# Kernel tuning notes

Hardware: AMD Instinct MI355X
Metric: run time of the kernel (lower is better)

## Reference

```python
import jax, jax.numpy as jnp
import numpy as np

# Bit-slice widths from SliceMethod([1,2,4]) on both input and weight sides
# (MSB-first, 7 magnitude bits total, sign carried per-element in each slice).
IN_SLICES = (1, 2, 4)
W_SLICES = (1, 2, 4)


def _l2norm(a):
    # F.normalize(a, p=2, dim=1)
    n = jnp.sqrt(jnp.sum(a * a, axis=1, keepdims=True))
    return a / jnp.maximum(n, 1e-12)


def _quantize(a, nbits):
    # symmetric fixed-point quantization to `nbits` magnitude bits,
    # dynamic per-tensor scale (bw_e=None -> fixed-point path)
    Q = float(2 ** nbits - 1)
    scale = jnp.max(jnp.abs(a))
    q = jnp.round(a / scale * Q)  # integer-valued float32 in [-Q, Q]
    return q, scale / Q


def _bit_slices(q, widths):
    # split |q| into bit groups (MSB-first per slice_method order); sign is
    # folded into each slice so recombination sum_k 2^off_k * slice_k == q
    sign = jnp.sign(q)
    mag = jnp.abs(q)
    total = sum(widths)
    slices = []
    off = total
    for w in widths:
        off -= w
        s = jnp.mod(jnp.floor(mag / (2.0 ** off)), 2.0 ** w)
        slices.append((sign * s, off))
    return slices


def setup_inputs() -> dict:
    key = jax.random.key(0)
    kx, kw = jax.random.split(key)
    x = jax.random.normal(kx, (4096, 1024), dtype=jnp.float32)
    weight = jax.random.normal(kw, (8192, 1024), dtype=jnp.float32)  # vectors.t -> [M, D]
    return {"x": x, "weight": weight}


def reference(x, weight):
    xn = _l2norm(x)        # [B, D]
    wn = _l2norm(weight)   # [M, D]
    qx, sx = _quantize(xn, sum(IN_SLICES))
    qw, sw = _quantize(wn, sum(W_SLICES))
    x_slices = _bit_slices(qx, IN_SLICES)
    w_slices = _bit_slices(qw, W_SLICES)
    # map_reduce_dot_func: 9 slice-pair low-bit GEMMs, recombined with 2^(oi+oj)
    acc = jnp.zeros((x.shape[0], weight.shape[0]), dtype=jnp.float32)
    for xs_k, ox in x_slices:
        for ws_k, ow in w_slices:
            acc = acc + (2.0 ** (ox + ow)) * jnp.einsum('bd,md->bm', xs_k, ws_k)
    cos = acc * sx * sw  # dequantize -> cosine similarity in [-1, 1]
    return 1.0 - cos
```

## Files before the change

### kernel.cpp

```cpp
#include <hip/hip_runtime.h>
#include <cstdint>
#include <cstddef>


#define D_COLS 1024
#define M_ROWS 4096
#define N_ROWS 8192

using i32x4 = __attribute__((ext_vector_type(4))) int;

__device__ __forceinline__ void gload_lds16(const void* g, void* lds) {
  __builtin_amdgcn_global_load_lds(
      (const __attribute__((address_space(1))) uint32_t*)g,
      (__attribute__((address_space(3))) uint32_t*)lds, 16, 0, 0);
}

__global__ __launch_bounds__(256) void rownorm_kernel(
    const float* __restrict__ x, const float* __restrict__ w,
    float* __restrict__ invnorm, float* __restrict__ rmax) {
  const int row = blockIdx.x;
  const float* a = (row < M_ROWS) ? x + (size_t)row * D_COLS
                                  : w + (size_t)(row - M_ROWS) * D_COLS;
  const float4 v = ((const float4*)a)[threadIdx.x];
  float ss = v.x * v.x + v.y * v.y + v.z * v.z + v.w * v.w;
  float mx = fmaxf(fmaxf(fabsf(v.x), fabsf(v.y)), fmaxf(fabsf(v.z), fabsf(v.w)));
#pragma unroll
  for (int off = 32; off; off >>= 1) {
    ss += __shfl_down(ss, off, 64);
    mx = fmaxf(mx, __shfl_down(mx, off, 64));
  }
  __shared__ float s_ss[4], s_mx[4];
  const int wave = threadIdx.x >> 6, lane = threadIdx.x & 63;
  if (lane == 0) { s_ss[wave] = ss; s_mx[wave] = mx; }
  __syncthreads();
  if (threadIdx.x == 0) {
    float tss = (s_ss[0] + s_ss[1]) + (s_ss[2] + s_ss[3]);
    float tmx = fmaxf(fmaxf(s_mx[0], s_mx[1]), fmaxf(s_mx[2], s_mx[3]));
    float inv = 1.0f / fmaxf(sqrtf(tss), 1e-12f);
    invnorm[row] = inv;
    rmax[row] = tmx * inv;
  }
}

__global__ __launch_bounds__(1024) void scale_reduce_kernel(
    const float* __restrict__ rmax, float* __restrict__ scales) {
  const int t = threadIdx.x;
  float mx = 0.f, mw = 0.f;
  for (int i = t; i < M_ROWS; i += 1024) mx = fmaxf(mx, rmax[i]);
  for (int i = t; i < N_ROWS; i += 1024) mw = fmaxf(mw, rmax[M_ROWS + i]);
#pragma unroll
  for (int off = 32; off; off >>= 1) {
    mx = fmaxf(mx, __shfl_down(mx, off, 64));
    mw = fmaxf(mw, __shfl_down(mw, off, 64));
  }
  __shared__ float smx[16], smw[16];
  const int wave = t >> 6, lane = t & 63;
  if (lane == 0) { smx[wave] = mx; smw[wave] = mw; }
  __syncthreads();
  if (t == 0) {
    float a = 0.f, b = 0.f;
#pragma unroll
    for (int i = 0; i < 16; ++i) { a = fmaxf(a, smx[i]); b = fmaxf(b, smw[i]); }
    scales[0] = a;
    scales[1] = b;
  }
}

__global__ __launch_bounds__(256) void quant_transpose_kernel(
    const float* __restrict__ a, const float* __restrict__ invnorm,
    const float* __restrict__ scale, uint4* __restrict__ img) {
  __shared__ uint4 T[128][16];
  const int t = threadIdx.x;
  const int g = blockIdx.x & 3;
  const int rh = (blockIdx.x >> 2) & 1;
  const int p = blockIdx.x >> 3;
  const float s = 127.0f / scale[0];

  const int cc_l = t & 15;
  const int tr = t >> 4;
#pragma unroll
  for (int rc = 0; rc < 8; ++rc) {
    const int rl = rc * 16 + tr;
    const int r = p * 256 + rh * 128 + rl;
    const float f = invnorm[r] * s;
    const float4* src = (const float4*)(a + (size_t)r * D_COLS + (g * 16 + cc_l) * 16);
    unsigned pk[4];
#pragma unroll
    for (int q = 0; q < 4; ++q) {
      const float4 v = src[q];
      const int q0 = (int)rintf(v.x * f), q1 = (int)rintf(v.y * f);
      const int q2 = (int)rintf(v.z * f), q3 = (int)rintf(v.w * f);
      pk[q] = (unsigned)(q0 & 0xff) | ((unsigned)(q1 & 0xff) << 8) |
              ((unsigned)(q2 & 0xff) << 16) | ((unsigned)(q3 & 0xff) << 24);
    }
    T[rl][cc_l ^ (rl & 15)] = make_uint4(pk[0], pk[1], pk[2], pk[3]);
  }
  __syncthreads();

  const int cc_w = t >> 4;
  const int rw = t & 15;
  uint4* dst = img + (size_t)p * 16384 + (size_t)(g * 16 + cc_w) * 256 + rh * 128;
#pragma unroll
  for (int i = 0; i < 8; ++i) {
    const int rl = i * 16 + rw;
    dst[rl] = T[rl][cc_w ^ (rl & 15)];
  }
}

__global__ __launch_bounds__(512, 2) void gemm_i8_kernel(
    const char* __restrict__ qx, const char* __restrict__ qw,
    const float* __restrict__ sx, const float* __restrict__ sw,
    float* __restrict__ out) {
  __shared__ __align__(16) char L[131072];
  const int t = threadIdx.x;
  const int wave = t >> 6, lane = t & 63;
  const int wr = wave >> 2, wc = wave & 3;
  const int rl = lane & 15, ko = lane >> 4;

  i32x4 acc[8][4] = {};

#define ISSUE_HT(h)                                                           \
  {                                                                           \
    const int kt_ = (h) >> 1, ks_ = (h) & 1, bb_ = (h) & 3;                   \
    const char* sa_ = qx + ((size_t)blockIdx.y * 8 + kt_) * 32768 + ks_ * 16384; \
    const char* sb_ = qw + ((size_t)blockIdx.x * 8 + kt_) * 32768 + ks_ * 16384; \
    _Pragma("unroll") for (int i_ = 0; i_ < 2; ++i_) {                        \
      gload_lds16(sa_ + wave * 2048 + i_ * 1024 + lane * 16,                  \
                  L + bb_ * 32768 + wave * 2048 + i_ * 1024);                 \
      gload_lds16(sb_ + wave * 2048 + i_ * 1024 + lane * 16,                  \
                  L + bb_ * 32768 + 16384 + wave * 2048 + i_ * 1024);         \
    }                                                                         \
  }

#define PHASE(h, VM)                                                          \
  {                                                                           \
    if ((h) + 3 < 16) ISSUE_HT((h) + 3);                                      \
    asm volatile("s_waitcnt vmcnt(" #VM ")" ::: "memory");                    \
    asm volatile("s_barrier" ::: "memory");                                   \
    const char* Ab_ = L + ((h) & 3) * 32768;                                  \
    const char* Bb_ = Ab_ + 16384;                                            \
    i32x4 af_[8], bf_[4];                                                     \
    _Pragma("unroll") for (int m_ = 0; m_ < 8; ++m_)                          \
      af_[m_] = *(const i32x4*)(Ab_ + (ko * 256 + wr * 128 + m_ * 16 + rl) * 16); \
    _Pragma("unroll") for (int n_ = 0; n_ < 4; ++n_)                          \
      bf_[n_] = *(const i32x4*)(Bb_ + (ko * 256 + wc * 64 + n_ * 16 + rl) * 16); \
    __builtin_amdgcn_s_setprio(1);                                            \
    _Pragma("unroll") for (int m_ = 0; m_ < 8; ++m_)                          \
      _Pragma("unroll") for (int n_ = 0; n_ < 4; ++n_)                        \
        acc[m_][n_] = __builtin_amdgcn_mfma_i32_16x16x64_i8(                  \
            af_[m_], bf_[n_], acc[m_][n_], 0, 0, 0);                          \
    __builtin_amdgcn_s_setprio(0);                                            \
    asm volatile("s_barrier" ::: "memory");                                   \
  }

  ISSUE_HT(0);
  ISSUE_HT(1);
  ISSUE_HT(2);

#pragma unroll 1
  for (int h = 0; h < 13; ++h) PHASE(h, 12);
  PHASE(13, 8);
  PHASE(14, 4);
  PHASE(15, 0);
#undef PHASE
#undef ISSUE_HT

  const float cs = sx[0] * sw[0] * (1.0f / 16129.0f);
  const int rowBase = blockIdx.y * 256;
  const int colBase = blockIdx.x * 256;
#pragma unroll
  for (int m = 0; m < 8; ++m) {
    const int row = rowBase + wr * 128 + m * 16 + ko * 4;
#pragma unroll
    for (int n = 0; n < 4; ++n) {
      const int col = colBase + wc * 64 + n * 16 + rl;
#pragma unroll
      for (int j = 0; j < 4; ++j)
        out[(size_t)(row + j) * N_ROWS + col] = 1.0f - (float)acc[m][n][j] * cs;
    }
  }
}

extern "C" void kernel_launch(void* const* d_in, const int* in_sizes, int n_in,
                              void* d_out, int out_size, void* d_ws, size_t ws_size,
                              hipStream_t stream) {
  const float* x = (const float*)d_in[0];
  const float* w = (const float*)d_in[1];
  float* out = (float*)d_out;

  char* ws = (char*)d_ws;
  char* qx = ws;
  char* qw = ws + (size_t)M_ROWS * D_COLS;
  float* invnorm = (float*)(ws + (size_t)(M_ROWS + N_ROWS) * D_COLS);
  float* rmax = invnorm + (M_ROWS + N_ROWS);
  float* scales = rmax + (M_ROWS + N_ROWS);

  rownorm_kernel<<<M_ROWS + N_ROWS, 256, 0, stream>>>(x, w, invnorm, rmax);
  scale_reduce_kernel<<<1, 1024, 0, stream>>>(rmax, scales);

  quant_transpose_kernel<<<M_ROWS / 256 * 8, 256, 0, stream>>>(
      x, invnorm, &scales[0], (uint4*)qx);
  quant_transpose_kernel<<<N_ROWS / 256 * 8, 256, 0, stream>>>(
      w, invnorm + M_ROWS, &scales[1], (uint4*)qw);

  dim3 grid(N_ROWS / 256, M_ROWS / 256);
  gemm_i8_kernel<<<grid, 512, 0, stream>>>(qx, qw, &scales[0], &scales[1], out);
}
```

Measured before the change: 80.82 us.

## Restructure int8 GEMM mainloop into double-buffered K-tiles with quarter-phase interleaving

Replaces the 4-deep ring of half-K-tiles with a 2-buffer scheme holding full 32KB K-tiles for A and B. Each K-tile is split into four phases that each issue half the MFMAs, and the next tile's global-to-LDS loads are spread across the first two phases. B fragments are reused across phase pairs and the min-waves-per-EU hint of 2 is dropped. The goal is to interleave loads with compute at finer granularity and cut register pressure. In exchange the prefetch depth drops to one tile, and the extra barriers per tile could expose memory latency.

Result: no change. 81.72 us (+1.1%).

```diff
diff --git a/kernel.cpp b/kernel.cpp
--- a/kernel.cpp
+++ b/kernel.cpp
@@ -107,7 +107,7 @@
   }
 }
 
-__global__ __launch_bounds__(512, 2) void gemm_i8_kernel(
+__global__ __launch_bounds__(512) void gemm_i8_kernel(
     const char* __restrict__ qx, const char* __restrict__ qw,
     const float* __restrict__ sx, const float* __restrict__ sw,
     float* __restrict__ out) {
@@ -119,51 +119,61 @@
 
   i32x4 acc[8][4] = {};
 
-#define ISSUE_HT(h)                                                           \
+#define ISSUE_PART(kt, part)                                                  \
   {                                                                           \
-    const int kt_ = (h) >> 1, ks_ = (h) & 1, bb_ = (h) & 3;                   \
-    const char* sa_ = qx + ((size_t)blockIdx.y * 8 + kt_) * 32768 + ks_ * 16384; \
-    const char* sb_ = qw + ((size_t)blockIdx.x * 8 + kt_) * 32768 + ks_ * 16384; \
-    _Pragma("unroll") for (int i_ = 0; i_ < 2; ++i_) {                        \
-      gload_lds16(sa_ + wave * 2048 + i_ * 1024 + lane * 16,                  \
-                  L + bb_ * 32768 + wave * 2048 + i_ * 1024);                 \
-      gload_lds16(sb_ + wave * 2048 + i_ * 1024 + lane * 16,                  \
-                  L + bb_ * 32768 + 16384 + wave * 2048 + i_ * 1024);         \
+    const char* sa_ = qx + ((size_t)blockIdx.y * 8 + (kt)) * 32768;           \
+    const char* sb_ = qw + ((size_t)blockIdx.x * 8 + (kt)) * 32768;           \
+    char* d_ = L + ((kt) & 1) * 65536;                                        \
+    _Pragma("unroll") for (int i_ = (part) * 2; i_ < (part) * 2 + 2; ++i_) {  \
+      gload_lds16(sa_ + wave * 4096 + i_ * 1024 + lane * 16,                  \
+                  d_ + wave * 4096 + i_ * 1024);                              \
+      gload_lds16(sb_ + wave * 4096 + i_ * 1024 + lane * 16,                  \
+                  d_ + 32768 + wave * 4096 + i_ * 1024);                      \
     }                                                                         \
   }
 
-#define PHASE(h, VM)                                                          \
+#define PHASE(kt, f)                                                          \
   {                                                                           \
-    if ((h) + 3 < 16) ISSUE_HT((h) + 3);                                      \
-    asm volatile("s_waitcnt vmcnt(" #VM ")" ::: "memory");                    \
-    asm volatile("s_barrier" ::: "memory");                                   \
-    const char* Ab_ = L + ((h) & 3) * 32768;                                  \
-    const char* Bb_ = Ab_ + 16384;                                            \
-    i32x4 af_[8], bf_[4];                                                     \
-    _Pragma("unroll") for (int m_ = 0; m_ < 8; ++m_)                          \
-      af_[m_] = *(const i32x4*)(Ab_ + (ko * 256 + wr * 128 + m_ * 16 + rl) * 16); \
-    _Pragma("unroll") for (int n_ = 0; n_ < 4; ++n_)                          \
-      bf_[n_] = *(const i32x4*)(Bb_ + (ko * 256 + wc * 64 + n_ * 16 + rl) * 16); \
+    const char* Ab_ = L + ((kt) & 1) * 65536;                                 \
+    const char* Bb_ = Ab_ + 32768;                                            \
+    const int kh_ = (f) >> 1, qm_ = (f) & 1;                                  \
+    i32x4 af_[4];                                                             \
+    _Pragma("unroll") for (int m_ = 0; m_ < 4; ++m_)                          \
+      af_[m_] = *(const i32x4*)(Ab_ +                                         \
+          ((kh_ * 4 + ko) * 256 + wr * 128 + qm_ * 64 + m_ * 16 + rl) * 16);  \
+    if ((f) % 2 == 0) {                                                       \
+      _Pragma("unroll") for (int n_ = 0; n_ < 4; ++n_)                        \
+        bf_[n_] = *(const i32x4*)(Bb_ +                                       \
+            ((kh_ * 4 + ko) * 256 + wc * 64 + n_ * 16 + rl) * 16);            \
+    }                                                                         \
+    if ((kt) < 7 && (f) < 2) ISSUE_PART((kt) + 1, (f));                       \
+    if ((f) == 3) asm volatile("s_waitcnt vmcnt(0)" ::: "memory");            \
+    __builtin_amdgcn_s_barrier();                                             \
+    asm volatile("s_waitcnt lgkmcnt(0)" ::: "memory");                        \
     __builtin_amdgcn_s_setprio(1);                                            \
-    _Pragma("unroll") for (int m_ = 0; m_ < 8; ++m_)                          \
+    _Pragma("unroll") for (int m_ = 0; m_ < 4; ++m_)                          \
       _Pragma("unroll") for (int n_ = 0; n_ < 4; ++n_)                        \
-        acc[m_][n_] = __builtin_amdgcn_mfma_i32_16x16x64_i8(                  \
-            af_[m_], bf_[n_], acc[m_][n_], 0, 0, 0);                          \
+        acc[qm_ * 4 + m_][n_] = __builtin_amdgcn_mfma_i32_16x16x64_i8(        \
+            af_[m_], bf_[n_], acc[qm_ * 4 + m_][n_], 0, 0, 0);                \
     __builtin_amdgcn_s_setprio(0);                                            \
-    asm volatile("s_barrier" ::: "memory");                                   \
-  }
-
-  ISSUE_HT(0);
-  ISSUE_HT(1);
-  ISSUE_HT(2);
+    __builtin_amdgcn_s_barrier();                                             \
+  }
+
+  ISSUE_PART(0, 0);
+  ISSUE_PART(0, 1);
+  asm volatile("s_waitcnt vmcnt(0)" ::: "memory");
+  __builtin_amdgcn_s_barrier();
 
 #pragma unroll 1
-  for (int h = 0; h < 13; ++h) PHASE(h, 12);
-  PHASE(13, 8);
-  PHASE(14, 4);
-  PHASE(15, 0);
+  for (int kt = 0; kt < 8; ++kt) {
+    i32x4 bf_[4];
+    PHASE(kt, 0);
+    PHASE(kt, 1);
+    PHASE(kt, 2);
+    PHASE(kt, 3);
+  }
 #undef PHASE
-#undef ISSUE_HT
+#undef ISSUE_PART
 
   const float cs = sx[0] * sw[0] * (1.0f / 16129.0f);
   const int rowBase = blockIdx.y * 256;
```

## Shrink GEMM tile to 128x128 with 4 waves, double buffering and XCD swizzle

Applied to the files above, without the earlier changes.

The int8 GEMM moves from 256x256 tiles with 8 waves and a 4-deep LDS ring (128KB) to 128x128 tiles with 4 waves and a 2-stage 32KB LDS buffer, aiming for 3 blocks per CU. The 1D grid of 2048 blocks is swizzled so consecutive block IDs spread across XCDs. The quant/transpose kernel's output layout is changed to match the new 128-row K-slab packing. Smaller tiles halve data reuse per block, raising global/L2 traffic, and the shallower prefetch exposes more load latency, in exchange for more blocks in flight.

Measured after the change: 88.13 us. +9.0%, slower.

```diff
diff --git a/kernel.cpp b/kernel.cpp
--- a/kernel.cpp
+++ b/kernel.cpp
@@ -72,8 +72,7 @@
   __shared__ uint4 T[128][16];
   const int t = threadIdx.x;
   const int g = blockIdx.x & 3;
-  const int rh = (blockIdx.x >> 2) & 1;
-  const int p = blockIdx.x >> 3;
+  const int Q = blockIdx.x >> 2;
   const float s = 127.0f / scale[0];
 
   const int cc_l = t & 15;
@@ -81,7 +80,7 @@
 #pragma unroll
   for (int rc = 0; rc < 8; ++rc) {
     const int rl = rc * 16 + tr;
-    const int r = p * 256 + rh * 128 + rl;
+    const int r = Q * 128 + rl;
     const float f = invnorm[r] * s;
     const float4* src = (const float4*)(a + (size_t)r * D_COLS + (g * 16 + cc_l) * 16);
     unsigned pk[4];
@@ -97,55 +96,64 @@
   }
   __syncthreads();
 
-  const int cc_w = t >> 4;
+  const int cc_w = g * 16 + (t >> 4);
   const int rw = t & 15;
-  uint4* dst = img + (size_t)p * 16384 + (size_t)(g * 16 + cc_w) * 256 + rh * 128;
+  uint4* dst = img + (size_t)(Q * 16 + (cc_w >> 2)) * 512 + (cc_w & 3) * 128;
 #pragma unroll
   for (int i = 0; i < 8; ++i) {
     const int rl = i * 16 + rw;
-    dst[rl] = T[rl][cc_w ^ (rl & 15)];
-  }
-}
-
-__global__ __launch_bounds__(512, 2) void gemm_i8_kernel(
+    dst[rl] = T[rl][(t >> 4) ^ (rl & 15)];
+  }
+}
+
+__global__ __launch_bounds__(256, 3) void gemm_i8_kernel(
     const char* __restrict__ qx, const char* __restrict__ qw,
     const float* __restrict__ sx, const float* __restrict__ sw,
     float* __restrict__ out) {
-  __shared__ __align__(16) char L[131072];
+  __shared__ __align__(16) char L[32768];
   const int t = threadIdx.x;
   const int wave = t >> 6, lane = t & 63;
-  const int wr = wave >> 2, wc = wave & 3;
+  const int wr = wave >> 1, wc = wave & 1;
   const int rl = lane & 15, ko = lane >> 4;
 
-  i32x4 acc[8][4] = {};
-
-#define ISSUE_HT(h)                                                           \
+  const int fid = blockIdx.x;
+  const int swz = (fid & 7) * 256 + (fid >> 3);
+  const int bx = swz & 63;
+  const int by = swz >> 6;
+
+  const char* sa0 = qx + (size_t)by * 16 * 8192;
+  const char* sb0 = qw + (size_t)bx * 16 * 8192;
+
+  i32x4 acc[4][4] = {};
+
+#define ISSUE_HT(ks)                                                          \
   {                                                                           \
-    const int kt_ = (h) >> 1, ks_ = (h) & 1, bb_ = (h) & 3;                   \
-    const char* sa_ = qx + ((size_t)blockIdx.y * 8 + kt_) * 32768 + ks_ * 16384; \
-    const char* sb_ = qw + ((size_t)blockIdx.x * 8 + kt_) * 32768 + ks_ * 16384; \
-    _Pragma("unroll") for (int i_ = 0; i_ < 2; ++i_) {                        \
-      gload_lds16(sa_ + wave * 2048 + i_ * 1024 + lane * 16,                  \
-                  L + bb_ * 32768 + wave * 2048 + i_ * 1024);                 \
-      gload_lds16(sb_ + wave * 2048 + i_ * 1024 + lane * 16,                  \
-                  L + bb_ * 32768 + 16384 + wave * 2048 + i_ * 1024);         \
-    }                                                                         \
-  }
-
-#define PHASE(h, VM)                                                          \
+    const char* sa_ = sa0 + (ks) * 8192;                                      \
+    const char* sb_ = sb0 + (ks) * 8192;                                      \
+    char* d_ = L + ((ks) & 1) * 16384;                                        \
+    gload_lds16(sa_ + wave * 2048 + lane * 16, d_ + wave * 2048);             \
+    gload_lds16(sa_ + wave * 2048 + 1024 + lane * 16, d_ + wave * 2048 + 1024); \
+    gload_lds16(sb_ + wave * 2048 + lane * 16, d_ + 8192 + wave * 2048);      \
+    gload_lds16(sb_ + wave * 2048 + 1024 + lane * 16,                         \
+                d_ + 8192 + wave * 2048 + 1024);                              \
+  }
+
+#define STEP(ks, VM)                                                          \
   {                                                                           \
-    if ((h) + 3 < 16) ISSUE_HT((h) + 3);                                      \
+    if ((ks) + 1 < 16) ISSUE_HT((ks) + 1);                                    \
     asm volatile("s_waitcnt vmcnt(" #VM ")" ::: "memory");                    \
     asm volatile("s_barrier" ::: "memory");                                   \
-    const char* Ab_ = L + ((h) & 3) * 32768;                                  \
-    const char* Bb_ = Ab_ + 16384;                                            \
-    i32x4 af_[8], bf_[4];                                                     \
-    _Pragma("unroll") for (int m_ = 0; m_ < 8; ++m_)                          \
-      af_[m_] = *(const i32x4*)(Ab_ + (ko * 256 + wr * 128 + m_ * 16 + rl) * 16); \
+    const char* Ab_ = L + ((ks) & 1) * 16384;                                 \
+    const char* Bb_ = Ab_ + 8192;                                             \
+    i32x4 af_[4], bf_[4];                                                     \
+    _Pragma("unroll") for (int m_ = 0; m_ < 4; ++m_)                          \
+      af_[m_] = *(const i32x4*)(Ab_ +                                         \
+          (ko * 128 + wr * 64 + m_ * 16 + rl) * 16);                          \
     _Pragma("unroll") for (int n_ = 0; n_ < 4; ++n_)                          \
-      bf_[n_] = *(const i32x4*)(Bb_ + (ko * 256 + wc * 64 + n_ * 16 + rl) * 16); \
+      bf_[n_] = *(const i32x4*)(Bb_ +                                         \
+          (ko * 128 + wc * 64 + n_ * 16 + rl) * 16);                          \
     __builtin_amdgcn_s_setprio(1);                                            \
-    _Pragma("unroll") for (int m_ = 0; m_ < 8; ++m_)                          \
+    _Pragma("unroll") for (int m_ = 0; m_ < 4; ++m_)                          \
       _Pragma("unroll") for (int n_ = 0; n_ < 4; ++n_)                        \
         acc[m_][n_] = __builtin_amdgcn_mfma_i32_16x16x64_i8(                  \
             af_[m_], bf_[n_], acc[m_][n_], 0, 0, 0);                          \
@@ -154,26 +162,22 @@
   }
 
   ISSUE_HT(0);
-  ISSUE_HT(1);
-  ISSUE_HT(2);
 
 #pragma unroll 1
-  for (int h = 0; h < 13; ++h) PHASE(h, 12);
-  PHASE(13, 8);
-  PHASE(14, 4);
-  PHASE(15, 0);
-#undef PHASE
+  for (int ks = 0; ks < 15; ++ks) STEP(ks, 4);
+  STEP(15, 0);
+#undef STEP
 #undef ISSUE_HT
 
   const float cs = sx[0] * sw[0] * (1.0f / 16129.0f);
-  const int rowBase = blockIdx.y * 256;
-  const int colBase = blockIdx.x * 256;
-#pragma unroll
-  for (int m = 0; m < 8; ++m) {
-    const int row = rowBase + wr * 128 + m * 16 + ko * 4;
+  const int rowBase = by * 128 + wr * 64;
+  const int colBase = bx * 128 + wc * 64;
+#pragma unroll
+  for (int m = 0; m < 4; ++m) {
+    const int row = rowBase + m * 16 + ko * 4;
 #pragma unroll
     for (int n = 0; n < 4; ++n) {
-      const int col = colBase + wc * 64 + n * 16 + rl;
+      const int col = colBase + n * 16 + rl;
 #pragma unroll
       for (int j = 0; j < 4; ++j)
         out[(size_t)(row + j) * N_ROWS + col] = 1.0f - (float)acc[m][n][j] * cs;
@@ -198,11 +202,10 @@
   rownorm_kernel<<<M_ROWS + N_ROWS, 256, 0, stream>>>(x, w, invnorm, rmax);
   scale_reduce_kernel<<<1, 1024, 0, stream>>>(rmax, scales);
 
-  quant_transpose_kernel<<<M_ROWS / 256 * 8, 256, 0, stream>>>(
+  quant_transpose_kernel<<<M_ROWS / 128 * 4, 256, 0, stream>>>(
       x, invnorm, &scales[0], (uint4*)qx);
-  quant_transpose_kernel<<<N_ROWS / 256 * 8, 256, 0, stream>>>(
+  quant_transpose_kernel<<<N_ROWS / 128 * 4, 256, 0, stream>>>(
       w, invnorm + M_ROWS, &scales[1], (uint4*)qw);
 
-  dim3 grid(N_ROWS / 256, M_ROWS / 256);
-  gemm_i8_kernel<<<grid, 512, 0, stream>>>(qx, qw, &scales[0], &scales[1], out);
-}
+  gemm_i8_kernel<<<dim3(2048), 256, 0, stream>>>(qx, qw, &scales[0], &scales[1], out);
+}
```
